# Kernel optimization log

Measured on AMD Instinct MI355X. Metric: run time of the kernel, lower is better.

## Reference

```python
import jax, jax.numpy as jnp
import numpy as np

TAU = 0.2
EPS = 1e-12  # torch F.normalize eps

def _l2norm(x):
    n = jnp.sqrt(jnp.sum(x * x, axis=-1, keepdims=True))
    return x / jnp.maximum(n, EPS)

def setup_inputs() -> dict:
    key = jax.random.key(0)
    k1, k2 = jax.random.split(key)
    B, Nx, Ny, D = 2, 8192, 8192, 128
    feat_x = jax.random.normal(k1, (B, Nx, D), dtype=jnp.float32)
    feat_y = jax.random.normal(k2, (B, Ny, D), dtype=jnp.float32)
    verts_mask_x = jnp.ones((B, Nx), dtype=jnp.float32)
    verts_mask_y = jnp.ones((B, Ny), dtype=jnp.float32)
    return {"feat_x": feat_x, "feat_y": feat_y, "verts_mask_x": verts_mask_x, "verts_mask_y": verts_mask_y}

def reference(feat_x, feat_y, verts_mask_x, verts_mask_y):
    # cosine similarity scores: [B, Nx, Ny]
    log_alpha = jnp.einsum('bxd,byd->bxy', _l2norm(feat_x), _l2norm(feat_y)) / TAU
    # stable softmax over last dim (normalise_dim = -1)
    alpha = jax.nn.softmax(log_alpha, axis=-1)
    # double masking: rows by mask_x, cols by mask_y
    return alpha * verts_mask_x[:, :, None] * verts_mask_y[:, None, :]
```

## Files before the change

### kernel.cpp

```cpp
#include <hip/hip_runtime.h>
#include <hip/hip_bf16.h>


typedef __attribute__((ext_vector_type(8))) short short8;
typedef __attribute__((ext_vector_type(4))) float float4v;

constexpr int B = 2, NX = 8192, NY = 8192, DD = 128;
constexpr int BM = 128, BN = 128;
constexpr int NSPLIT = 8;
constexpr int YCHUNK = NY / NSPLIT;
constexpr int ROWB = 256;
constexpr float TAU_INV = 5.0f;

__device__ __forceinline__ void gload16(const void* g, void* l) {
    __builtin_amdgcn_global_load_lds(
        (const __attribute__((address_space(1))) void*)g,
        (__attribute__((address_space(3))) void*)l, 16, 0, 0);
}

__device__ __forceinline__ void stage_tile(const char* gsrc, char* lds, int wid, int lane) {
    const int srow = wid * 32;
    const int lr4 = lane >> 4;
    const int lcb = (lane & 15) * 16;
#pragma unroll
    for (int i = 0; i < 8; ++i) {
        int row = srow + i * 4 + lr4;
        int scb = lcb ^ ((row & 7) << 4);
        gload16(gsrc + (size_t)row * ROWB + scb, lds + (srow + i * 4) * ROWB);
    }
}

__global__ __launch_bounds__(256) void l2norm_kernel(const float* __restrict__ in,
                                                     __hip_bfloat16* __restrict__ out,
                                                     int rows) {
    int wid = threadIdx.x >> 6, lane = threadIdx.x & 63;
    int row = blockIdx.x * 4 + wid;
    if (row >= rows) return;
    float2 v = ((const float2*)(in + (size_t)row * DD))[lane];
    float ss = v.x * v.x + v.y * v.y;
#pragma unroll
    for (int off = 32; off >= 1; off >>= 1) ss += __shfl_xor(ss, off);
    float inv = 1.0f / fmaxf(sqrtf(ss), 1e-12f);
    __hip_bfloat162 o;
    o.x = __float2bfloat16(v.x * inv);
    o.y = __float2bfloat16(v.y * inv);
    ((__hip_bfloat162*)(out + (size_t)row * DD))[lane] = o;
}

__global__ __launch_bounds__(256) void pass1_kernel(const __hip_bfloat16* __restrict__ Xn,
                                                    const __hip_bfloat16* __restrict__ Yn,
                                                    float* __restrict__ partial) {
    __shared__ __hip_bfloat16 Xs[BM][DD];
    __shared__ __hip_bfloat16 Ys[BN][DD];
    const int split = blockIdx.x, xt = blockIdx.y, b = blockIdx.z;
    const int t = threadIdx.x;
    const int lane = t & 63, wid = t >> 6;
    const int wm = wid >> 1, wn = wid & 1;
    const int lrow = lane & 15, lhi = lane >> 4;

    stage_tile((const char*)(Xn + (size_t)(b * NX + xt * BM) * DD), (char*)&Xs[0][0], wid, lane);

    float run[4][4];
#pragma unroll
    for (int m = 0; m < 4; ++m)
#pragma unroll
        for (int r = 0; r < 4; ++r) run[m][r] = 0.f;

    for (int tile = 0; tile < YCHUNK / BN; ++tile) {
        __syncthreads();
        stage_tile((const char*)(Yn + (size_t)(b * NY + split * YCHUNK + tile * BN) * DD),
                   (char*)&Ys[0][0], wid, lane);
        __syncthreads();

        float4v acc[4][4];
#pragma unroll
        for (int m = 0; m < 4; ++m)
#pragma unroll
            for (int n = 0; n < 4; ++n) acc[m][n] = (float4v)(0.f);
#pragma unroll
        for (int kk = 0; kk < 4; ++kk) {
            const int cb = (kk * 64 + lhi * 16) ^ ((lrow & 7) << 4);
            short8 a[4], bb[4];
#pragma unroll
            for (int m = 0; m < 4; ++m)
                a[m] = *(const short8*)((const char*)Xs + (size_t)(wm * 64 + m * 16 + lrow) * ROWB + cb);
#pragma unroll
            for (int n = 0; n < 4; ++n)
                bb[n] = *(const short8*)((const char*)Ys + (size_t)(wn * 64 + n * 16 + lrow) * ROWB + cb);
#pragma unroll
            for (int m = 0; m < 4; ++m)
#pragma unroll
                for (int n = 0; n < 4; ++n)
                    acc[m][n] = __builtin_amdgcn_mfma_f32_16x16x32_bf16(a[m], bb[n], acc[m][n], 0, 0, 0);
        }
#pragma unroll
        for (int m = 0; m < 4; ++m)
#pragma unroll
            for (int r = 0; r < 4; ++r) {
                float s = 0.f;
#pragma unroll
                for (int n = 0; n < 4; ++n) s += __expf(acc[m][n][r] * TAU_INV);
                run[m][r] += s;
            }
    }

#pragma unroll
    for (int m = 0; m < 4; ++m)
#pragma unroll
        for (int r = 0; r < 4; ++r) {
            float v = run[m][r];
            v += __shfl_xor(v, 1);
            v += __shfl_xor(v, 2);
            v += __shfl_xor(v, 4);
            v += __shfl_xor(v, 8);
            run[m][r] = v;
        }

    __syncthreads();
    float* lred = (float*)Ys;
    if (lrow == 0) {
#pragma unroll
        for (int m = 0; m < 4; ++m)
#pragma unroll
            for (int r = 0; r < 4; ++r) {
                int xl = wm * 64 + m * 16 + lhi * 4 + r;
                lred[wn * BM + xl] = run[m][r];
            }
    }
    __syncthreads();
    if (t < BM) {
        float tot = lred[t] + lred[BM + t];
        partial[(size_t)split * (B * NX) + (size_t)b * NX + xt * BM + t] = tot;
    }
}

__global__ void combine_kernel(const float* __restrict__ partial,
                               const float* __restrict__ maskx,
                               float* __restrict__ rowscale) {
    int idx = blockIdx.x * 256 + threadIdx.x;
    if (idx >= B * NX) return;
    float s = 0.f;
#pragma unroll
    for (int i = 0; i < NSPLIT; ++i) s += partial[(size_t)i * (B * NX) + idx];
    rowscale[idx] = maskx[idx] / s;
}

__global__ __launch_bounds__(256) void pass2_kernel(const __hip_bfloat16* __restrict__ Xn,
                                                    const __hip_bfloat16* __restrict__ Yn,
                                                    const float* __restrict__ rowscale,
                                                    const float* __restrict__ masky,
                                                    float* __restrict__ out) {
    __shared__ char smem[65536];
    char* XsB = smem;
    char* YsB = smem + 32768;
    const int yt = blockIdx.x, xt = blockIdx.y, b = blockIdx.z;
    const int t = threadIdx.x;
    const int lane = t & 63, wid = t >> 6;
    const int wy = wid >> 1, wx = wid & 1;
    const int lrow = lane & 15, lhi = lane >> 4;

    stage_tile((const char*)(Xn + (size_t)(b * NX + xt * BM) * DD), XsB, wid, lane);
    stage_tile((const char*)(Yn + (size_t)(b * NY + yt * BN) * DD), YsB, wid, lane);
    __syncthreads();

    float4v acc[4][4];
#pragma unroll
    for (int n = 0; n < 4; ++n)
#pragma unroll
        for (int m = 0; m < 4; ++m) acc[n][m] = (float4v)(0.f);

#pragma unroll
    for (int kk = 0; kk < 4; ++kk) {
        const int cb = (kk * 64 + lhi * 16) ^ ((lrow & 7) << 4);
        short8 a[4], bb[4];
#pragma unroll
        for (int n = 0; n < 4; ++n)
            a[n] = *(const short8*)(YsB + (size_t)(wy * 64 + n * 16 + lrow) * ROWB + cb);
#pragma unroll
        for (int m = 0; m < 4; ++m)
            bb[m] = *(const short8*)(XsB + (size_t)(wx * 64 + m * 16 + lrow) * ROWB + cb);
#pragma unroll
        for (int n = 0; n < 4; ++n)
#pragma unroll
            for (int m = 0; m < 4; ++m)
                acc[n][m] = __builtin_amdgcn_mfma_f32_16x16x32_bf16(a[n], bb[m], acc[n][m], 0, 0, 0);
    }

    const int ybase = yt * BN + wy * 64;
    const int xbase = xt * BM + wx * 64;

    float rs[4];
#pragma unroll
    for (int m = 0; m < 4; ++m)
        rs[m] = rowscale[(size_t)b * NX + xbase + m * 16 + lrow];
    float4v my4[4];
#pragma unroll
    for (int n = 0; n < 4; ++n)
        my4[n] = *(const float4v*)(masky + (size_t)b * NY + ybase + n * 16 + lhi * 4);

    __syncthreads();

#pragma unroll
    for (int m = 0; m < 4; ++m) {
        const int xl = wx * 64 + m * 16 + lrow;
#pragma unroll
        for (int n = 0; n < 4; ++n) {
            float4v o;
#pragma unroll
            for (int r = 0; r < 4; ++r)
                o[r] = __expf(acc[n][m][r] * TAU_INV) * rs[m] * my4[n][r];
            const int yb = wy * 256 + n * 64 + lhi * 16;
            *(float4v*)(smem + (size_t)xl * 512 + (yb ^ ((xl & 7) << 4))) = o;
        }
    }
    __syncthreads();

    const int halfl = lane >> 5, l31 = lane & 31;
    const size_t orow0 = ((size_t)b * NX + xt * BM) * NY + yt * BN;
#pragma unroll
    for (int s = 0; s < 16; ++s) {
        const int xr = wid * 32 + s * 2 + halfl;
        float4v v = *(const float4v*)(smem + (size_t)xr * 512 + ((l31 * 16) ^ ((xr & 7) << 4)));
        *(float4v*)(out + orow0 + (size_t)xr * NY + l31 * 4) = v;
    }
}

extern "C" void kernel_launch(void* const* d_in, const int* in_sizes, int n_in,
                              void* d_out, int out_size, void* d_ws, size_t ws_size,
                              hipStream_t stream) {
    const float* feat_x = (const float*)d_in[0];
    const float* feat_y = (const float*)d_in[1];
    const float* maskx  = (const float*)d_in[2];
    const float* masky  = (const float*)d_in[3];
    float* out = (float*)d_out;

    char* ws = (char*)d_ws;
    __hip_bfloat16* Xn = (__hip_bfloat16*)ws;
    __hip_bfloat16* Yn = (__hip_bfloat16*)(ws + (size_t)B * NX * DD * 2);
    float* partial  = (float*)(ws + (size_t)B * (NX + NY) * DD * 2);
    float* rowscale = partial + (size_t)NSPLIT * B * NX;

    l2norm_kernel<<<B * NX / 4, 256, 0, stream>>>(feat_x, Xn, B * NX);
    l2norm_kernel<<<B * NY / 4, 256, 0, stream>>>(feat_y, Yn, B * NY);
    pass1_kernel<<<dim3(NSPLIT, NX / BM, B), 256, 0, stream>>>(Xn, Yn, partial);
    combine_kernel<<<(B * NX + 255) / 256, 256, 0, stream>>>(partial, maskx, rowscale);
    pass2_kernel<<<dim3(NY / BN, NX / BM, B), 256, 0, stream>>>(Xn, Yn, rowscale, masky, out);
}
```

Measured before the change: 176.1 us.

## Loop pass2 over eight Y tiles per block with prefetch and direct stores

Each pass2 block now keeps its X tile resident and walks eight consecutive Y tiles. The next Y tile is prefetched into LDS via global_load_lds while the current tile's exp/scale results are written straight to global memory. The LDS transpose stage for output is removed, and masky is staged once into LDS. This cuts repeated X tile loads and block launch overhead and overlaps loads with stores. In exchange, stores are now 16-byte scattered per lane rather than coalesced full rows, and the grid shrinks by a factor of eight.

```diff
diff --git a/kernel.cpp b/kernel.cpp
--- a/kernel.cpp
+++ b/kernel.cpp
@@ -9,6 +9,8 @@
 constexpr int BM = 128, BN = 128;
 constexpr int NSPLIT = 8;
 constexpr int YCHUNK = NY / NSPLIT;
+constexpr int NTILE2 = 8;
+constexpr int YT2 = NTILE2 * BN;
 constexpr int ROWB = 256;
 constexpr float TAU_INV = 5.0f;
 
@@ -150,78 +152,87 @@
                                                     const float* __restrict__ rowscale,
                                                     const float* __restrict__ masky,
                                                     float* __restrict__ out) {
-    __shared__ char smem[65536];
+    __shared__ char smem[32768 + 32768 + 4096];
     char* XsB = smem;
     char* YsB = smem + 32768;
+    char* MsB = smem + 65536;
     const int yt = blockIdx.x, xt = blockIdx.y, b = blockIdx.z;
     const int t = threadIdx.x;
     const int lane = t & 63, wid = t >> 6;
     const int wy = wid >> 1, wx = wid & 1;
     const int lrow = lane & 15, lhi = lane >> 4;
 
+    const char* gy = (const char*)(Yn + (size_t)(b * NY + yt * YT2) * DD);
+
     stage_tile((const char*)(Xn + (size_t)(b * NX + xt * BM) * DD), XsB, wid, lane);
-    stage_tile((const char*)(Yn + (size_t)(b * NY + yt * BN) * DD), YsB, wid, lane);
+    stage_tile(gy, YsB, wid, lane);
+    gload16((const char*)(masky + (size_t)b * NY + yt * YT2) + wid * 1024 + lane * 16,
+            MsB + wid * 1024);
+    float rs[4];
+#pragma unroll
+    for (int m = 0; m < 4; ++m)
+        rs[m] = rowscale[(size_t)b * NX + xt * BM + wx * 64 + m * 16 + lrow];
     __syncthreads();
 
-    float4v acc[4][4];
-#pragma unroll
-    for (int n = 0; n < 4; ++n)
-#pragma unroll
-        for (int m = 0; m < 4; ++m) acc[n][m] = (float4v)(0.f);
-
-#pragma unroll
-    for (int kk = 0; kk < 4; ++kk) {
-        const int cb = (kk * 64 + lhi * 16) ^ ((lrow & 7) << 4);
-        short8 a[4], bb[4];
+    const int xbase = xt * BM + wx * 64;
+
+#pragma unroll
+    for (int tt = 0; tt < NTILE2; ++tt) {
+        float4v acc[4][4];
 #pragma unroll
         for (int n = 0; n < 4; ++n)
-            a[n] = *(const short8*)(YsB + (size_t)(wy * 64 + n * 16 + lrow) * ROWB + cb);
-#pragma unroll
-        for (int m = 0; m < 4; ++m)
-            bb[m] = *(const short8*)(XsB + (size_t)(wx * 64 + m * 16 + lrow) * ROWB + cb);
+#pragma unroll
+            for (int m = 0; m < 4; ++m) acc[n][m] = (float4v)(0.f);
+#pragma unroll
+        for (int kk = 0; kk < 4; ++kk) {
+            const int cb = (kk * 64 + lhi * 16) ^ ((lrow & 7) << 4);
+            short8 a[4], bb[4];
+#pragma unroll
+            for (int n = 0; n < 4; ++n)
+                a[n] = *(const short8*)(YsB + (size_t)(wy * 64 + n * 16 + lrow) * ROWB + cb);
+#pragma unroll
+            for (int m = 0; m < 4; ++m)
+                bb[m] = *(const short8*)(XsB + (size_t)(wx * 64 + m * 16 + lrow) * ROWB + cb);
+#pragma unroll
+            for (int n = 0; n < 4; ++n)
+#pragma unroll
+                for (int m = 0; m < 4; ++m)
+                    acc[n][m] = __builtin_amdgcn_mfma_f32_16x16x32_bf16(a[n], bb[m], acc[n][m], 0, 0, 0);
+        }
+        float4v my4[4];
 #pragma unroll
         for (int n = 0; n < 4; ++n)
-#pragma unroll
-            for (int m = 0; m < 4; ++m)
-                acc[n][m] = __builtin_amdgcn_mfma_f32_16x16x32_bf16(a[n], bb[m], acc[n][m], 0, 0, 0);
-    }
-
-    const int ybase = yt * BN + wy * 64;
-    const int xbase = xt * BM + wx * 64;
-
-    float rs[4];
-#pragma unroll
-    for (int m = 0; m < 4; ++m)
-        rs[m] = rowscale[(size_t)b * NX + xbase + m * 16 + lrow];
-    float4v my4[4];
-#pragma unroll
-    for (int n = 0; n < 4; ++n)
-        my4[n] = *(const float4v*)(masky + (size_t)b * NY + ybase + n * 16 + lhi * 4);
-
-    __syncthreads();
-
-#pragma unroll
-    for (int m = 0; m < 4; ++m) {
-        const int xl = wx * 64 + m * 16 + lrow;
-#pragma unroll
-        for (int n = 0; n < 4; ++n) {
-            float4v o;
-#pragma unroll
-            for (int r = 0; r < 4; ++r)
-                o[r] = __expf(acc[n][m][r] * TAU_INV) * rs[m] * my4[n][r];
-            const int yb = wy * 256 + n * 64 + lhi * 16;
-            *(float4v*)(smem + (size_t)xl * 512 + (yb ^ ((xl & 7) << 4))) = o;
-        }
-    }
-    __syncthreads();
-
-    const int halfl = lane >> 5, l31 = lane & 31;
-    const size_t orow0 = ((size_t)b * NX + xt * BM) * NY + yt * BN;
-#pragma unroll
-    for (int s = 0; s < 16; ++s) {
-        const int xr = wid * 32 + s * 2 + halfl;
-        float4v v = *(const float4v*)(smem + (size_t)xr * 512 + ((l31 * 16) ^ ((xr & 7) << 4)));
-        *(float4v*)(out + orow0 + (size_t)xr * NY + l31 * 4) = v;
+            my4[n] = *(const float4v*)(MsB + tt * 512 + wy * 256 + n * 64 + lhi * 16);
+
+        __builtin_amdgcn_sched_barrier(0);
+        __builtin_amdgcn_s_barrier();
+        __builtin_amdgcn_sched_barrier(0);
+
+        if (tt + 1 < NTILE2)
+            stage_tile(gy + (size_t)(tt + 1) * BN * ROWB, YsB, wid, lane);
+        __builtin_amdgcn_sched_barrier(0);
+
+#pragma unroll
+        for (int m = 0; m < 4; ++m) {
+            const int x = xbase + m * 16 + lrow;
+            float* orow = out + ((size_t)b * NX + x) * NY + yt * YT2 + tt * BN;
+#pragma unroll
+            for (int n = 0; n < 4; ++n) {
+                float4v o;
+#pragma unroll
+                for (int r = 0; r < 4; ++r)
+                    o[r] = __expf(acc[n][m][r] * TAU_INV) * rs[m] * my4[n][r];
+                *(float4v*)(orow + wy * 64 + n * 16 + lhi * 4) = o;
+            }
+        }
+        __builtin_amdgcn_sched_barrier(0);
+
+        if (tt + 1 < NTILE2) {
+            asm volatile("s_waitcnt vmcnt(16)" ::: "memory");
+            __builtin_amdgcn_sched_barrier(0);
+            __builtin_amdgcn_s_barrier();
+            __builtin_amdgcn_sched_barrier(0);
+        }
     }
 }
 
@@ -244,5 +255,5 @@
     l2norm_kernel<<<B * NY / 4, 256, 0, stream>>>(feat_y, Yn, B * NY);
     pass1_kernel<<<dim3(NSPLIT, NX / BM, B), 256, 0, stream>>>(Xn, Yn, partial);
     combine_kernel<<<(B * NX + 255) / 256, 256, 0, stream>>>(partial, maskx, rowscale);
-    pass2_kernel<<<dim3(NY / BN, NX / BM, B), 256, 0, stream>>>(Xn, Yn, rowscale, masky, out);
-}
+    pass2_kernel<<<dim3(NY / YT2, NX / BM, B), 256, 0, stream>>>(Xn, Yn, rowscale, masky, out);
+}
```

Measured after the change: 240.8 us. +36.7%, slower.

## Triple-buffer Y tiles in pass1 with async LDS loads and partial waitcnt

Applied to the files above, without the earlier changes.

Pass1 now streams Y in 64-row tiles through a three-slot LDS ring buffer, prefetching two tiles ahead with global_load_lds. It waits with a partial vmcnt and a single barrier per tile instead of two full syncthreads, so loads overlap the MFMA and exp work. Pass2 interleaves the X and Y staging loads in one loop. The smaller tile halves MFMA work per barrier, which could reduce efficiency, and the hand-counted vmcnt values depend on each wave issuing exactly four loads per tile.

```diff
diff --git a/kernel.cpp b/kernel.cpp
--- a/kernel.cpp
+++ b/kernel.cpp
@@ -7,8 +7,10 @@
 
 constexpr int B = 2, NX = 8192, NY = 8192, DD = 128;
 constexpr int BM = 128, BN = 128;
+constexpr int BN1 = 64;
 constexpr int NSPLIT = 8;
 constexpr int YCHUNK = NY / NSPLIT;
+constexpr int NT1 = YCHUNK / BN1;
 constexpr int ROWB = 256;
 constexpr float TAU_INV = 5.0f;
 
@@ -18,15 +20,17 @@
         (__attribute__((address_space(3))) void*)l, 16, 0, 0);
 }
 
-__device__ __forceinline__ void stage_tile(const char* gsrc, char* lds, int wid, int lane) {
-    const int srow = wid * 32;
+template<int NR>
+__device__ __forceinline__ void stage_rows(const char* gsrc, char* lds, int wid, int lane) {
+    constexpr int RPW = NR / 4;
+    const int srow = wid * RPW;
     const int lr4 = lane >> 4;
     const int lcb = (lane & 15) * 16;
 #pragma unroll
-    for (int i = 0; i < 8; ++i) {
-        int row = srow + i * 4 + lr4;
+    for (int i = 0; i < RPW; i += 4) {
+        int row = srow + i + lr4;
         int scb = lcb ^ ((row & 7) << 4);
-        gload16(gsrc + (size_t)row * ROWB + scb, lds + (srow + i * 4) * ROWB);
+        gload16(gsrc + (size_t)row * ROWB + scb, lds + (size_t)(srow + i) * ROWB);
     }
 }
 
@@ -50,15 +54,21 @@
 __global__ __launch_bounds__(256) void pass1_kernel(const __hip_bfloat16* __restrict__ Xn,
                                                     const __hip_bfloat16* __restrict__ Yn,
                                                     float* __restrict__ partial) {
-    __shared__ __hip_bfloat16 Xs[BM][DD];
-    __shared__ __hip_bfloat16 Ys[BN][DD];
+    __shared__ char Xs[BM * ROWB];
+    __shared__ char Ys[3][BN1 * ROWB];
     const int split = blockIdx.x, xt = blockIdx.y, b = blockIdx.z;
     const int t = threadIdx.x;
     const int lane = t & 63, wid = t >> 6;
     const int wm = wid >> 1, wn = wid & 1;
     const int lrow = lane & 15, lhi = lane >> 4;
 
-    stage_tile((const char*)(Xn + (size_t)(b * NX + xt * BM) * DD), (char*)&Xs[0][0], wid, lane);
+    const char* gy0 = (const char*)(Yn + (size_t)(b * NY + split * YCHUNK) * DD);
+
+    stage_rows<BM>((const char*)(Xn + (size_t)(b * NX + xt * BM) * DD), Xs, wid, lane);
+    stage_rows<BN1>(gy0, Ys[0], wid, lane);
+    stage_rows<BN1>(gy0 + (size_t)BN1 * ROWB, Ys[1], wid, lane);
+    asm volatile("s_waitcnt vmcnt(4)" ::: "memory");
+    __builtin_amdgcn_s_barrier();
 
     float run[4][4];
 #pragma unroll
@@ -66,42 +76,49 @@
 #pragma unroll
         for (int r = 0; r < 4; ++r) run[m][r] = 0.f;
 
-    for (int tile = 0; tile < YCHUNK / BN; ++tile) {
-        __syncthreads();
-        stage_tile((const char*)(Yn + (size_t)(b * NY + split * YCHUNK + tile * BN) * DD),
-                   (char*)&Ys[0][0], wid, lane);
-        __syncthreads();
-
-        float4v acc[4][4];
-#pragma unroll
-        for (int m = 0; m < 4; ++m)
-#pragma unroll
-            for (int n = 0; n < 4; ++n) acc[m][n] = (float4v)(0.f);
+#pragma unroll
+    for (int tile = 0; tile < NT1; ++tile) {
+        if (tile + 2 < NT1)
+            stage_rows<BN1>(gy0 + (size_t)(tile + 2) * BN1 * ROWB,
+                            Ys[(tile + 2) % 3], wid, lane);
+
+        const char* ycur = Ys[tile % 3];
+        float4v acc[4][2];
+#pragma unroll
+        for (int m = 0; m < 4; ++m)
+#pragma unroll
+            for (int n = 0; n < 2; ++n) acc[m][n] = (float4v)(0.f);
 #pragma unroll
         for (int kk = 0; kk < 4; ++kk) {
             const int cb = (kk * 64 + lhi * 16) ^ ((lrow & 7) << 4);
-            short8 a[4], bb[4];
+            short8 a[4], bb[2];
 #pragma unroll
             for (int m = 0; m < 4; ++m)
-                a[m] = *(const short8*)((const char*)Xs + (size_t)(wm * 64 + m * 16 + lrow) * ROWB + cb);
-#pragma unroll
-            for (int n = 0; n < 4; ++n)
-                bb[n] = *(const short8*)((const char*)Ys + (size_t)(wn * 64 + n * 16 + lrow) * ROWB + cb);
+                a[m] = *(const short8*)(Xs + (size_t)(wm * 64 + m * 16 + lrow) * ROWB + cb);
+#pragma unroll
+            for (int n = 0; n < 2; ++n)
+                bb[n] = *(const short8*)(ycur + (size_t)(wn * 32 + n * 16 + lrow) * ROWB + cb);
 #pragma unroll
             for (int m = 0; m < 4; ++m)
 #pragma unroll
-                for (int n = 0; n < 4; ++n)
+                for (int n = 0; n < 2; ++n)
                     acc[m][n] = __builtin_amdgcn_mfma_f32_16x16x32_bf16(a[m], bb[n], acc[m][n], 0, 0, 0);
         }
 #pragma unroll
         for (int m = 0; m < 4; ++m)
 #pragma unroll
             for (int r = 0; r < 4; ++r) {
-                float s = 0.f;
-#pragma unroll
-                for (int n = 0; n < 4; ++n) s += __expf(acc[m][n][r] * TAU_INV);
+                float s = __expf(acc[m][0][r] * TAU_INV) + __expf(acc[m][1][r] * TAU_INV);
                 run[m][r] += s;
             }
+
+        if (tile + 1 < NT1) {
+            if (tile + 2 < NT1)
+                asm volatile("s_waitcnt vmcnt(4)" ::: "memory");
+            else
+                asm volatile("s_waitcnt vmcnt(0)" ::: "memory");
+            __builtin_amdgcn_s_barrier();
+        }
     }
 
 #pragma unroll
@@ -117,7 +134,7 @@
         }
 
     __syncthreads();
-    float* lred = (float*)Ys;
+    float* lred = (float*)Xs;
     if (lrow == 0) {
 #pragma unroll
         for (int m = 0; m < 4; ++m)
@@ -159,8 +176,20 @@
     const int wy = wid >> 1, wx = wid & 1;
     const int lrow = lane & 15, lhi = lane >> 4;
 
-    stage_tile((const char*)(Xn + (size_t)(b * NX + xt * BM) * DD), XsB, wid, lane);
-    stage_tile((const char*)(Yn + (size_t)(b * NY + yt * BN) * DD), YsB, wid, lane);
+    {
+        const int srow = wid * 32;
+        const int lr4 = lane >> 4;
+        const int lcb = (lane & 15) * 16;
+        const char* gx = (const char*)(Xn + (size_t)(b * NX + xt * BM) * DD);
+        const char* gy = (const char*)(Yn + (size_t)(b * NY + yt * BN) * DD);
+#pragma unroll
+        for (int i = 0; i < 8; ++i) {
+            int row = srow + i * 4 + lr4;
+            int scb = lcb ^ ((row & 7) << 4);
+            gload16(gx + (size_t)row * ROWB + scb, XsB + (srow + i * 4) * ROWB);
+            gload16(gy + (size_t)row * ROWB + scb, YsB + (srow + i * 4) * ROWB);
+        }
+    }
     __syncthreads();
 
     float4v acc[4][4];
```

Result: slower. 198.1 us (+12.5%).
